# Kernel optimization log

Measured on AMD Instinct MI355X. Metric: run time of the kernel, lower is better.

The kernel has to match this reference:

```python
import jax, jax.numpy as jnp
import numpy as np

OC, IC = 11008, 4096
B, S = 32, 1
OUTLIER_FRACTION = 0.05


def setup_inputs() -> dict:
    key = jax.random.key(0)
    k1, k2, k3, k4 = jax.random.split(key, 4)
    x = jax.random.normal(k1, (B, S, IC), dtype=jnp.float32)
    weight = jax.random.normal(k2, (OC, IC), dtype=jnp.float32) * 0.02
    bias = jax.random.normal(k3, (OC,), dtype=jnp.float32) * 0.02
    outlier_mask = jax.random.uniform(k4, (OC, IC)) < OUTLIER_FRACTION
    return {"x": x, "weight": weight, "bias": bias, "outlier_mask": outlier_mask}


def _xnor_quant_weight(w, outlier_mask):
    # XnorBinaryLinear.quant_weight(outlier_mask=...): zero outliers, per-row
    # detached scale = mean|w|, center rows, sign() with STE clip path.
    wz = jnp.where(outlier_mask, 0.0, w)
    scale = jax.lax.stop_gradient(jnp.mean(jnp.abs(wz), axis=-1, keepdims=True))  # [OC,1]
    wc = wz - jnp.mean(wz, axis=-1, keepdims=True)  # centered rows
    clipped = jnp.clip(wc, -1.0, 1.0)
    # value = scale*sign(wc); gradient flows through clipped (STE)
    return jax.lax.stop_gradient(scale * jnp.sign(wc) - clipped) + clipped


def reference(x, weight, bias, outlier_mask):
    wq = _xnor_quant_weight(weight, outlier_mask)
    # binarize_except_outliers: keep full-precision weight at outlier positions
    w_eff = jnp.where(outlier_mask, weight, wq)  # [OC,IC]
    # F.linear(x, w, b) = x @ w.T + b
    return jnp.einsum("bsi,oi->bso", x, w_eff) + bias
```

## Files before the change

### kernel.cpp

```cpp
#include <hip/hip_runtime.h>
#include <stdint.h>


#define OC 11008
#define IC 4096
#define BATCH 32
#define SKM 8
#define SKF 4

typedef __attribute__((ext_vector_type(8))) short short8;
typedef __attribute__((ext_vector_type(4))) float floatx4;
typedef __attribute__((ext_vector_type(4))) int intx4;

static __device__ __forceinline__ unsigned short f2bf(float f) {
  uint32_t u = __builtin_bit_cast(uint32_t, f);
  uint32_t r = (u + 0x7fffu + ((u >> 16) & 1u)) >> 16;
  return (unsigned short)r;
}

__global__ __launch_bounds__(256) void fuse_kernel(
    const float* __restrict__ w, const int* __restrict__ mask,
    const float* __restrict__ x, unsigned short* __restrict__ weff,
    unsigned short* __restrict__ xbf) {
  const int blk = blockIdx.x;
  const int t = threadIdx.x;
  const int lane = t & 63;
  const int wvid = t >> 6;

  if (blk < 8) {
    const int b = blk * 4 + wvid;
    const float* xr = x + (size_t)b * IC;
    unsigned short* xo = xbf + (size_t)b * IC;
#pragma unroll
    for (int q = 0; q < 16; ++q) {
      const int i = (q << 8) + (lane << 2);
      const float4 v = *reinterpret_cast<const float4*>(xr + i);
      ushort4 u;
      u.x = f2bf(v.x); u.y = f2bf(v.y); u.z = f2bf(v.z); u.w = f2bf(v.w);
      *reinterpret_cast<ushort4*>(xo + i) = u;
    }
    return;
  }

  const int row = (blk - 8) * 4 + wvid;
  const float* wr = w + (size_t)row * IC;
  const int* mr = mask + (size_t)row * IC;

  float4 wv[16];
  uint32_t bits_lo = 0, bits_hi = 0;
  float s1 = 0.f, s2 = 0.f;
#pragma unroll
  for (int q = 0; q < 16; ++q) {
    const int i = (q << 8) + (lane << 2);
    wv[q] = *reinterpret_cast<const float4*>(wr + i);
    const intx4 mv =
        __builtin_nontemporal_load(reinterpret_cast<const intx4*>(mr + i));
    const uint32_t nb = (uint32_t)(mv.x != 0) | ((uint32_t)(mv.y != 0) << 1) |
                        ((uint32_t)(mv.z != 0) << 2) |
                        ((uint32_t)(mv.w != 0) << 3);
    if (q < 8)
      bits_lo |= nb << (q * 4);
    else
      bits_hi |= nb << ((q - 8) * 4);
    const float z0 = (nb & 1u) ? 0.f : wv[q].x;
    const float z1 = (nb & 2u) ? 0.f : wv[q].y;
    const float z2 = (nb & 4u) ? 0.f : wv[q].z;
    const float z3 = (nb & 8u) ? 0.f : wv[q].w;
    s1 += z0 + z1 + z2 + z3;
    s2 += fabsf(z0) + fabsf(z1) + fabsf(z2) + fabsf(z3);
  }

#pragma unroll
  for (int off = 1; off < 64; off <<= 1) {
    s1 += __shfl_xor(s1, off);
    s2 += __shfl_xor(s2, off);
  }
  const float mean = s1 * (1.0f / IC);
  const float scale = s2 * (1.0f / IC);

  unsigned short* wo = weff + (size_t)row * IC;
#pragma unroll
  for (int q = 0; q < 16; ++q) {
    const uint32_t nb =
        ((q < 8) ? (bits_lo >> (q * 4)) : (bits_hi >> ((q - 8) * 4))) & 0xFu;
    float4 v = wv[q];
    v.x = (nb & 1u) ? v.x : copysignf(scale, v.x - mean);
    v.y = (nb & 2u) ? v.y : copysignf(scale, v.y - mean);
    v.z = (nb & 4u) ? v.z : copysignf(scale, v.z - mean);
    v.w = (nb & 8u) ? v.w : copysignf(scale, v.w - mean);
    ushort4 u;
    u.x = f2bf(v.x); u.y = f2bf(v.y); u.z = f2bf(v.z); u.w = f2bf(v.w);
    *reinterpret_cast<ushort4*>(wo + (q << 8) + (lane << 2)) = u;
  }
}

__global__ __launch_bounds__(256) void mfma_kernel(
    const unsigned short* __restrict__ weff,
    const unsigned short* __restrict__ xbf, float* __restrict__ part) {
  const int bx = blockIdx.x;
  const int tile = bx >> 3;
  const int sk = bx & 7;
  const int t = threadIdx.x;
  const int wv = t >> 6;
  const int l = t & 63;
  const int l15 = l & 15, l4 = l >> 4;

  const int o = tile * 64 + wv * 16 + l15;
  const int k0 = sk * (IC / SKM) + l4 * 8;

  const unsigned short* bp = weff + (size_t)o * IC + k0;
  const unsigned short* ap0 = xbf + (size_t)l15 * IC + k0;
  const unsigned short* ap1 = xbf + (size_t)(16 + l15) * IC + k0;

  floatx4 acc0 = {0.f, 0.f, 0.f, 0.f};
  floatx4 acc1 = {0.f, 0.f, 0.f, 0.f};
#pragma unroll 4
  for (int kk = 0; kk < (IC / SKM) / 32; ++kk) {
    const short8 bf = *reinterpret_cast<const short8*>(bp + kk * 32);
    const short8 a0 = *reinterpret_cast<const short8*>(ap0 + kk * 32);
    const short8 a1 = *reinterpret_cast<const short8*>(ap1 + kk * 32);
    acc0 = __builtin_amdgcn_mfma_f32_16x16x32_bf16(a0, bf, acc0, 0, 0, 0);
    acc1 = __builtin_amdgcn_mfma_f32_16x16x32_bf16(a1, bf, acc1, 0, 0, 0);
  }

  float* pb = part + (size_t)sk * (BATCH * OC);
#pragma unroll
  for (int r = 0; r < 4; ++r) {
    const int b0 = l4 * 4 + r;
    pb[(size_t)b0 * OC + o] = acc0[r];
    pb[(size_t)(b0 + 16) * OC + o] = acc1[r];
  }
}

__global__ __launch_bounds__(256) void reduce_kernel(
    const float* __restrict__ part, const float* __restrict__ bias,
    float* __restrict__ out, int nsk) {
  const int idx = blockIdx.x * 256 + threadIdx.x;
  if (idx < BATCH * OC) {
    const int o = idx % OC;
    float v = bias[o];
    for (int sk = 0; sk < nsk; ++sk) v += part[(size_t)sk * (BATCH * OC) + idx];
    out[idx] = v;
  }
}

__global__ __launch_bounds__(256) void stats_kernel_fb(
    const int* __restrict__ mask, const float* __restrict__ w,
    float2* __restrict__ stats) {
  const int o = blockIdx.x;
  const int t = threadIdx.x;
  const float* wr = w + (size_t)o * IC;
  const int* mr = mask + (size_t)o * IC;
  float s1 = 0.f, s2 = 0.f;
#pragma unroll
  for (int q = 0; q < 4; ++q) {
    const int i = (q << 10) + (t << 2);
    const float4 wv = *reinterpret_cast<const float4*>(wr + i);
    const int4 mv = *reinterpret_cast<const int4*>(mr + i);
    const float z0 = mv.x ? 0.f : wv.x, z1 = mv.y ? 0.f : wv.y;
    const float z2 = mv.z ? 0.f : wv.z, z3 = mv.w ? 0.f : wv.w;
    s1 += z0 + z1 + z2 + z3;
    s2 += fabsf(z0) + fabsf(z1) + fabsf(z2) + fabsf(z3);
  }
#pragma unroll
  for (int off = 32; off > 0; off >>= 1) {
    s1 += __shfl_down(s1, off);
    s2 += __shfl_down(s2, off);
  }
  __shared__ float r1[4], r2[4];
  if ((t & 63) == 0) { r1[t >> 6] = s1; r2[t >> 6] = s2; }
  __syncthreads();
  if (t == 0)
    stats[o] = make_float2((r1[0] + r1[1] + r1[2] + r1[3]) * (1.0f / IC),
                           (r2[0] + r2[1] + r2[2] + r2[3]) * (1.0f / IC));
}

__global__ __launch_bounds__(256) void gemv_kernel_fb(
    const float* __restrict__ x, const float* __restrict__ w,
    const int* __restrict__ mask, const float2* __restrict__ stats,
    float* __restrict__ part) {
  const int bx = blockIdx.x;
  const int tile = bx >> 2;
  const int sk = bx & 3;
  const int t = threadIdx.x;
  const int wvid = t >> 6;
  const int lane = t & 63;
  const int il = lane & 15;
  const int bg = lane >> 4;
  const int row0 = tile * 32 + wvid * 8;
  const int i0 = sk * (IC / SKF);
  const float* wr0 = w + (size_t)row0 * IC;
  const int* mk0 = mask + (size_t)row0 * IC;
  const float* xb = x + (size_t)(bg * 8) * IC;

  float2 stv[8];
#pragma unroll
  for (int r = 0; r < 8; ++r) stv[r] = stats[row0 + r];
  float acc[8][8];
#pragma unroll
  for (int r = 0; r < 8; ++r)
#pragma unroll
    for (int j = 0; j < 8; ++j) acc[r][j] = 0.f;

  for (int s_ = 0; s_ < (IC / SKF) / 64; ++s_) {
    const int i = i0 + (s_ << 6) + (il << 2);
    float4 wf[8];
#pragma unroll
    for (int r = 0; r < 8; ++r) {
      wf[r] = *reinterpret_cast<const float4*>(wr0 + (size_t)r * IC + i);
      const int4 mv = *reinterpret_cast<const int4*>(mk0 + (size_t)r * IC + i);
      const float m = stv[r].x, sc = stv[r].y;
      wf[r].x = mv.x ? wf[r].x : copysignf(sc, wf[r].x - m);
      wf[r].y = mv.y ? wf[r].y : copysignf(sc, wf[r].y - m);
      wf[r].z = mv.z ? wf[r].z : copysignf(sc, wf[r].z - m);
      wf[r].w = mv.w ? wf[r].w : copysignf(sc, wf[r].w - m);
    }
#pragma unroll
    for (int j = 0; j < 8; ++j) {
      const float4 xv = *reinterpret_cast<const float4*>(xb + (size_t)j * IC + i);
#pragma unroll
      for (int r = 0; r < 8; ++r)
        acc[r][j] += wf[r].x * xv.x + wf[r].y * xv.y + wf[r].z * xv.z +
                     wf[r].w * xv.w;
    }
  }
#pragma unroll
  for (int off = 8; off >= 1; off >>= 1)
#pragma unroll
    for (int r = 0; r < 8; ++r)
#pragma unroll
      for (int j = 0; j < 8; ++j) acc[r][j] += __shfl_xor(acc[r][j], off);
  if (il == 0)
#pragma unroll
    for (int r = 0; r < 8; ++r)
#pragma unroll
      for (int j = 0; j < 8; ++j)
        part[(size_t)sk * (BATCH * OC) + (size_t)(bg * 8 + j) * OC +
             (row0 + r)] = acc[r][j];
}

extern "C" void kernel_launch(void* const* d_in, const int* in_sizes, int n_in,
                              void* d_out, int out_size, void* d_ws,
                              size_t ws_size, hipStream_t stream) {
  const float* x = (const float*)d_in[0];
  const float* w = (const float*)d_in[1];
  const float* bias = (const float*)d_in[2];
  const int* mask = (const int*)d_in[3];
  float* out = (float*)d_out;

  const size_t weff_b = (size_t)OC * IC * 2;
  const size_t xbf_b = (size_t)BATCH * IC * 2;
  const size_t part_b = (size_t)SKM * BATCH * OC * 4;

  if (ws_size >= weff_b + xbf_b + part_b) {
    unsigned short* weff = (unsigned short*)d_ws;
    unsigned short* xbf = (unsigned short*)((char*)d_ws + weff_b);
    float* part = (float*)((char*)d_ws + weff_b + xbf_b);

    fuse_kernel<<<8 + OC / 4, 256, 0, stream>>>(w, mask, x, weff, xbf);
    mfma_kernel<<<(OC / 64) * SKM, 256, 0, stream>>>(weff, xbf, part);
    reduce_kernel<<<(BATCH * OC + 255) / 256, 256, 0, stream>>>(part, bias, out,
                                                                SKM);
  } else {
    float2* stats = (float2*)d_ws;
    float* part = (float*)((char*)d_ws + (size_t)OC * sizeof(float2));
    stats_kernel_fb<<<OC, 256, 0, stream>>>(mask, w, stats);
    gemv_kernel_fb<<<(OC / 32) * SKF, 256, 0, stream>>>(x, w, mask, stats, part);
    reduce_kernel<<<(BATCH * OC + 255) / 256, 256, 0, stream>>>(part, bias, out,
                                                                SKF);
  }
}
```

Measured before the change: 112.4 us.

## Process one weight row per 1024-thread block with shared-memory row reduction

```diff
diff --git a/kernel.cpp b/kernel.cpp
--- a/kernel.cpp
+++ b/kernel.cpp
@@ -10,7 +10,6 @@
 
 typedef __attribute__((ext_vector_type(8))) short short8;
 typedef __attribute__((ext_vector_type(4))) float floatx4;
-typedef __attribute__((ext_vector_type(4))) int intx4;
 
 static __device__ __forceinline__ unsigned short f2bf(float f) {
   uint32_t u = __builtin_bit_cast(uint32_t, f);
@@ -18,80 +17,63 @@
   return (unsigned short)r;
 }
 
-__global__ __launch_bounds__(256) void fuse_kernel(
+__global__ __launch_bounds__(1024) void fuse_kernel(
     const float* __restrict__ w, const int* __restrict__ mask,
     const float* __restrict__ x, unsigned short* __restrict__ weff,
     unsigned short* __restrict__ xbf) {
   const int blk = blockIdx.x;
   const int t = threadIdx.x;
-  const int lane = t & 63;
-  const int wvid = t >> 6;
-
-  if (blk < 8) {
-    const int b = blk * 4 + wvid;
-    const float* xr = x + (size_t)b * IC;
-    unsigned short* xo = xbf + (size_t)b * IC;
-#pragma unroll
-    for (int q = 0; q < 16; ++q) {
-      const int i = (q << 8) + (lane << 2);
-      const float4 v = *reinterpret_cast<const float4*>(xr + i);
-      ushort4 u;
-      u.x = f2bf(v.x); u.y = f2bf(v.y); u.z = f2bf(v.z); u.w = f2bf(v.w);
-      *reinterpret_cast<ushort4*>(xo + i) = u;
-    }
+  const int i = t << 2;
+
+  if (blk < BATCH) {
+    const float* xr = x + (size_t)blk * IC;
+    unsigned short* xo = xbf + (size_t)blk * IC;
+    const float4 v = *reinterpret_cast<const float4*>(xr + i);
+    ushort4 u;
+    u.x = f2bf(v.x); u.y = f2bf(v.y); u.z = f2bf(v.z); u.w = f2bf(v.w);
+    *reinterpret_cast<ushort4*>(xo + i) = u;
     return;
   }
 
-  const int row = (blk - 8) * 4 + wvid;
+  const int row = blk - BATCH;
   const float* wr = w + (size_t)row * IC;
   const int* mr = mask + (size_t)row * IC;
 
-  float4 wv[16];
-  uint32_t bits_lo = 0, bits_hi = 0;
-  float s1 = 0.f, s2 = 0.f;
-#pragma unroll
-  for (int q = 0; q < 16; ++q) {
-    const int i = (q << 8) + (lane << 2);
-    wv[q] = *reinterpret_cast<const float4*>(wr + i);
-    const intx4 mv =
-        __builtin_nontemporal_load(reinterpret_cast<const intx4*>(mr + i));
-    const uint32_t nb = (uint32_t)(mv.x != 0) | ((uint32_t)(mv.y != 0) << 1) |
-                        ((uint32_t)(mv.z != 0) << 2) |
-                        ((uint32_t)(mv.w != 0) << 3);
-    if (q < 8)
-      bits_lo |= nb << (q * 4);
-    else
-      bits_hi |= nb << ((q - 8) * 4);
-    const float z0 = (nb & 1u) ? 0.f : wv[q].x;
-    const float z1 = (nb & 2u) ? 0.f : wv[q].y;
-    const float z2 = (nb & 4u) ? 0.f : wv[q].z;
-    const float z3 = (nb & 8u) ? 0.f : wv[q].w;
-    s1 += z0 + z1 + z2 + z3;
-    s2 += fabsf(z0) + fabsf(z1) + fabsf(z2) + fabsf(z3);
-  }
+  const float4 wv = *reinterpret_cast<const float4*>(wr + i);
+  const int4 mv = *reinterpret_cast<const int4*>(mr + i);
+  const uint32_t nb = (uint32_t)(mv.x != 0) | ((uint32_t)(mv.y != 0) << 1) |
+                      ((uint32_t)(mv.z != 0) << 2) |
+                      ((uint32_t)(mv.w != 0) << 3);
+  const float z0 = (nb & 1u) ? 0.f : wv.x;
+  const float z1 = (nb & 2u) ? 0.f : wv.y;
+  const float z2 = (nb & 4u) ? 0.f : wv.z;
+  const float z3 = (nb & 8u) ? 0.f : wv.w;
+  float s1 = z0 + z1 + z2 + z3;
+  float s2 = fabsf(z0) + fabsf(z1) + fabsf(z2) + fabsf(z3);
 
 #pragma unroll
   for (int off = 1; off < 64; off <<= 1) {
     s1 += __shfl_xor(s1, off);
     s2 += __shfl_xor(s2, off);
   }
-  const float mean = s1 * (1.0f / IC);
-  const float scale = s2 * (1.0f / IC);
-
-  unsigned short* wo = weff + (size_t)row * IC;
-#pragma unroll
-  for (int q = 0; q < 16; ++q) {
-    const uint32_t nb =
-        ((q < 8) ? (bits_lo >> (q * 4)) : (bits_hi >> ((q - 8) * 4))) & 0xFu;
-    float4 v = wv[q];
-    v.x = (nb & 1u) ? v.x : copysignf(scale, v.x - mean);
-    v.y = (nb & 2u) ? v.y : copysignf(scale, v.y - mean);
-    v.z = (nb & 4u) ? v.z : copysignf(scale, v.z - mean);
-    v.w = (nb & 8u) ? v.w : copysignf(scale, v.w - mean);
-    ushort4 u;
-    u.x = f2bf(v.x); u.y = f2bf(v.y); u.z = f2bf(v.z); u.w = f2bf(v.w);
-    *reinterpret_cast<ushort4*>(wo + (q << 8) + (lane << 2)) = u;
-  }
+  __shared__ float red[16][2];
+  const int wvid = t >> 6;
+  if ((t & 63) == 0) { red[wvid][0] = s1; red[wvid][1] = s2; }
+  __syncthreads();
+  float a = 0.f, b = 0.f;
+#pragma unroll
+  for (int k = 0; k < 16; ++k) { a += red[k][0]; b += red[k][1]; }
+  const float mean = a * (1.0f / IC);
+  const float scale = b * (1.0f / IC);
+
+  float4 v = wv;
+  v.x = (nb & 1u) ? v.x : copysignf(scale, v.x - mean);
+  v.y = (nb & 2u) ? v.y : copysignf(scale, v.y - mean);
+  v.z = (nb & 4u) ? v.z : copysignf(scale, v.z - mean);
+  v.w = (nb & 8u) ? v.w : copysignf(scale, v.w - mean);
+  ushort4 u;
+  u.x = f2bf(v.x); u.y = f2bf(v.y); u.z = f2bf(v.z); u.w = f2bf(v.w);
+  *reinterpret_cast<ushort4*>(weff + (size_t)row * IC + i) = u;
 }
 
 __global__ __launch_bounds__(256) void mfma_kernel(
@@ -257,7 +239,7 @@
     unsigned short* xbf = (unsigned short*)((char*)d_ws + weff_b);
     float* part = (float*)((char*)d_ws + weff_b + xbf_b);
 
-    fuse_kernel<<<8 + OC / 4, 256, 0, stream>>>(w, mask, x, weff, xbf);
+    fuse_kernel<<<BATCH + OC, 1024, 0, stream>>>(w, mask, x, weff, xbf);
     mfma_kernel<<<(OC / 64) * SKM, 256, 0, stream>>>(weff, xbf, part);
     reduce_kernel<<<(BATCH * OC + 255) / 256, 256, 0, stream>>>(part, bias, out,
                                                                 SKM);
```

Result: slower. 118.9 us (+5.8%).

## Split weight into packed sign bits plus sparse outlier corrections

Applied to the files above, without the earlier changes.

```diff
diff --git a/kernel.cpp b/kernel.cpp
--- a/kernel.cpp
+++ b/kernel.cpp
@@ -7,61 +7,75 @@
 #define BATCH 32
 #define SKM 8
 #define SKF 4
+#define CAP 512
 
 typedef __attribute__((ext_vector_type(8))) short short8;
 typedef __attribute__((ext_vector_type(4))) float floatx4;
-typedef __attribute__((ext_vector_type(4))) int intx4;
+typedef __attribute__((ext_vector_type(4))) unsigned int uintx4;
 
 static __device__ __forceinline__ unsigned short f2bf(float f) {
   uint32_t u = __builtin_bit_cast(uint32_t, f);
   uint32_t r = (u + 0x7fffu + ((u >> 16) & 1u)) >> 16;
   return (unsigned short)r;
 }
-
-__global__ __launch_bounds__(256) void fuse_kernel(
-    const float* __restrict__ w, const int* __restrict__ mask,
-    const float* __restrict__ x, unsigned short* __restrict__ weff,
-    unsigned short* __restrict__ xbf) {
+static __device__ __forceinline__ float bf2f(unsigned short h) {
+  uint32_t u = ((uint32_t)h) << 16;
+  return __builtin_bit_cast(float, u);
+}
+
+__global__ __launch_bounds__(256) void xprep_kernel(
+    const float* __restrict__ x, unsigned short* __restrict__ xbf,
+    unsigned short* __restrict__ xT) {
   const int blk = blockIdx.x;
   const int t = threadIdx.x;
-  const int lane = t & 63;
-  const int wvid = t >> 6;
-
-  if (blk < 8) {
-    const int b = blk * 4 + wvid;
+  if (blk < 64) {
+    const int i = blk * 64 + (t >> 2);
+    const int b0 = (t & 3) * 8;
+    unsigned short tmp[8];
+#pragma unroll
+    for (int j = 0; j < 8; ++j) tmp[j] = f2bf(x[(size_t)(b0 + j) * IC + i]);
+    *reinterpret_cast<short8*>(xT + (size_t)i * BATCH + b0) =
+        *reinterpret_cast<short8*>(tmp);
+  } else {
+    const int b = blk - 64;
     const float* xr = x + (size_t)b * IC;
     unsigned short* xo = xbf + (size_t)b * IC;
 #pragma unroll
-    for (int q = 0; q < 16; ++q) {
-      const int i = (q << 8) + (lane << 2);
+    for (int q = 0; q < 4; ++q) {
+      const int i = (q << 10) + (t << 2);
       const float4 v = *reinterpret_cast<const float4*>(xr + i);
       ushort4 u;
       u.x = f2bf(v.x); u.y = f2bf(v.y); u.z = f2bf(v.z); u.w = f2bf(v.w);
       *reinterpret_cast<ushort4*>(xo + i) = u;
     }
-    return;
-  }
-
-  const int row = (blk - 8) * 4 + wvid;
+  }
+}
+
+__global__ __launch_bounds__(256) void fuse2_kernel(
+    const float* __restrict__ w, const int* __restrict__ mask,
+    unsigned long long* __restrict__ signs, float* __restrict__ scaleArr,
+    int* __restrict__ countArr, uint32_t* __restrict__ corrArr) {
+  const int blk = blockIdx.x;
+  const int t = threadIdx.x;
+  const int lane = t & 63;
+  const int wvid = t >> 6;
+  const int row = blk * 4 + wvid;
+
   const float* wr = w + (size_t)row * IC;
   const int* mr = mask + (size_t)row * IC;
 
   float4 wv[16];
-  uint32_t bits_lo = 0, bits_hi = 0;
+  unsigned long long mb = 0;
   float s1 = 0.f, s2 = 0.f;
 #pragma unroll
   for (int q = 0; q < 16; ++q) {
     const int i = (q << 8) + (lane << 2);
     wv[q] = *reinterpret_cast<const float4*>(wr + i);
-    const intx4 mv =
-        __builtin_nontemporal_load(reinterpret_cast<const intx4*>(mr + i));
+    const int4 mv = *reinterpret_cast<const int4*>(mr + i);
     const uint32_t nb = (uint32_t)(mv.x != 0) | ((uint32_t)(mv.y != 0) << 1) |
                         ((uint32_t)(mv.z != 0) << 2) |
                         ((uint32_t)(mv.w != 0) << 3);
-    if (q < 8)
-      bits_lo |= nb << (q * 4);
-    else
-      bits_hi |= nb << ((q - 8) * 4);
+    mb |= (unsigned long long)nb << (q * 4);
     const float z0 = (nb & 1u) ? 0.f : wv[q].x;
     const float z1 = (nb & 2u) ? 0.f : wv[q].y;
     const float z2 = (nb & 4u) ? 0.f : wv[q].z;
@@ -77,26 +91,47 @@
   }
   const float mean = s1 * (1.0f / IC);
   const float scale = s2 * (1.0f / IC);
-
-  unsigned short* wo = weff + (size_t)row * IC;
+  if (lane == 0) scaleArr[row] = scale;
+
+  unsigned long long sb = 0;
 #pragma unroll
   for (int q = 0; q < 16; ++q) {
-    const uint32_t nb =
-        ((q < 8) ? (bits_lo >> (q * 4)) : (bits_hi >> ((q - 8) * 4))) & 0xFu;
-    float4 v = wv[q];
-    v.x = (nb & 1u) ? v.x : copysignf(scale, v.x - mean);
-    v.y = (nb & 2u) ? v.y : copysignf(scale, v.y - mean);
-    v.z = (nb & 4u) ? v.z : copysignf(scale, v.z - mean);
-    v.w = (nb & 8u) ? v.w : copysignf(scale, v.w - mean);
-    ushort4 u;
-    u.x = f2bf(v.x); u.y = f2bf(v.y); u.z = f2bf(v.z); u.w = f2bf(v.w);
-    *reinterpret_cast<ushort4*>(wo + (q << 8) + (lane << 2)) = u;
+    sb |= (unsigned long long)(wv[q].x < mean) << (q * 4 + 0);
+    sb |= (unsigned long long)(wv[q].y < mean) << (q * 4 + 1);
+    sb |= (unsigned long long)(wv[q].z < mean) << (q * 4 + 2);
+    sb |= (unsigned long long)(wv[q].w < mean) << (q * 4 + 3);
+  }
+  signs[(size_t)row * 64 + lane] = sb;
+
+  int cnt = __popcll(mb);
+  int pref = cnt;
+#pragma unroll
+  for (int d = 1; d < 64; d <<= 1) {
+    int v = __shfl_up(pref, d);
+    if (lane >= d) pref += v;
+  }
+  if (lane == 63) countArr[row] = (pref < CAP) ? pref : CAP;
+  int pos = pref - cnt;
+  unsigned long long mm = mb;
+  while (mm) {
+    const int b = __ffsll(mm) - 1;
+    mm &= mm - 1;
+    const int q = b >> 2, e = b & 3;
+    const int idx = (q << 8) + (lane << 2) + e;
+    const float val = wr[idx];
+    const float sg = (val < mean) ? -scale : scale;
+    const float corr = val - sg;
+    if (pos < CAP)
+      corrArr[(size_t)row * CAP + pos] =
+          ((uint32_t)idx << 16) | (uint32_t)f2bf(corr);
+    ++pos;
   }
 }
 
 __global__ __launch_bounds__(256) void mfma_kernel(
-    const unsigned short* __restrict__ weff,
-    const unsigned short* __restrict__ xbf, float* __restrict__ part) {
+    const unsigned long long* __restrict__ signs,
+    const float* __restrict__ scaleArr, const unsigned short* __restrict__ xbf,
+    float* __restrict__ part) {
   const int bx = blockIdx.x;
   const int tile = bx >> 3;
   const int sk = bx & 7;
@@ -108,15 +143,29 @@
   const int o = tile * 64 + wv * 16 + l15;
   const int k0 = sk * (IC / SKM) + l4 * 8;
 
-  const unsigned short* bp = weff + (size_t)o * IC + k0;
+  const unsigned long long* sgp = signs + (size_t)o * 64;
   const unsigned short* ap0 = xbf + (size_t)l15 * IC + k0;
   const unsigned short* ap1 = xbf + (size_t)(16 + l15) * IC + k0;
+  const float scl = scaleArr[o];
 
   floatx4 acc0 = {0.f, 0.f, 0.f, 0.f};
   floatx4 acc1 = {0.f, 0.f, 0.f, 0.f};
-#pragma unroll 4
-  for (int kk = 0; kk < (IC / SKM) / 32; ++kk) {
-    const short8 bf = *reinterpret_cast<const short8*>(bp + kk * 32);
+#pragma unroll
+  for (int kk = 0; kk < 16; ++kk) {
+    const int k = k0 + kk * 32;
+    const int l_src = (k & 255) >> 2;
+    const int sh = (k >> 8) * 4;
+    const unsigned long long s0 = sgp[l_src];
+    const unsigned long long s1v = sgp[l_src + 1];
+    const uint32_t bits8 = ((uint32_t)(s0 >> sh) & 0xFu) |
+                           (((uint32_t)(s1v >> sh) & 0xFu) << 4);
+    uintx4 pr;
+#pragma unroll
+    for (int p = 0; p < 4; ++p) {
+      pr[p] = (((bits8 >> (2 * p)) & 1u) ? 0xBF80u : 0x3F80u) |
+              (((bits8 >> (2 * p + 1)) & 1u) ? 0xBF800000u : 0x3F800000u);
+    }
+    const short8 bf = __builtin_bit_cast(short8, pr);
     const short8 a0 = *reinterpret_cast<const short8*>(ap0 + kk * 32);
     const short8 a1 = *reinterpret_cast<const short8*>(ap1 + kk * 32);
     acc0 = __builtin_amdgcn_mfma_f32_16x16x32_bf16(a0, bf, acc0, 0, 0, 0);
@@ -127,8 +176,49 @@
 #pragma unroll
   for (int r = 0; r < 4; ++r) {
     const int b0 = l4 * 4 + r;
-    pb[(size_t)b0 * OC + o] = acc0[r];
-    pb[(size_t)(b0 + 16) * OC + o] = acc1[r];
+    pb[(size_t)b0 * OC + o] = acc0[r] * scl;
+    pb[(size_t)(b0 + 16) * OC + o] = acc1[r] * scl;
+  }
+}
+
+__global__ __launch_bounds__(256) void sparse_kernel(
+    const uint32_t* __restrict__ corrArr, const int* __restrict__ countArr,
+    const unsigned short* __restrict__ xT, float* __restrict__ part) {
+  __shared__ float lds[4][64][33];
+  const int t = threadIdx.x;
+  const int lane = t & 63;
+  const int wvid = t >> 6;
+  const int row = blockIdx.x * 4 + wvid;
+
+  const int cnt = countArr[row];
+  float acc[32];
+#pragma unroll
+  for (int b = 0; b < 32; ++b) acc[b] = 0.f;
+
+  for (int j = lane; j < cnt; j += 64) {
+    const uint32_t p = corrArr[(size_t)row * CAP + j];
+    const int idx = p >> 16;
+    const float cv = bf2f((unsigned short)(p & 0xFFFFu));
+    const unsigned short* xr = xT + (size_t)idx * BATCH;
+    const short8 h0 = *reinterpret_cast<const short8*>(xr);
+    const short8 h1 = *reinterpret_cast<const short8*>(xr + 8);
+    const short8 h2 = *reinterpret_cast<const short8*>(xr + 16);
+    const short8 h3 = *reinterpret_cast<const short8*>(xr + 24);
+#pragma unroll
+    for (int e = 0; e < 8; ++e) {
+      acc[e] += cv * bf2f((unsigned short)h0[e]);
+      acc[8 + e] += cv * bf2f((unsigned short)h1[e]);
+      acc[16 + e] += cv * bf2f((unsigned short)h2[e]);
+      acc[24 + e] += cv * bf2f((unsigned short)h3[e]);
+    }
+  }
+
+#pragma unroll
+  for (int b = 0; b < 32; ++b) lds[wvid][lane][b] = acc[b];
+  if (lane < 32) {
+    float s = 0.f;
+    for (int l2 = 0; l2 < 64; ++l2) s += lds[wvid][l2][lane];
+    part[(size_t)SKM * (BATCH * OC) + (size_t)lane * OC + row] = s;
   }
 }
 
@@ -248,19 +338,33 @@
   const int* mask = (const int*)d_in[3];
   float* out = (float*)d_out;
 
-  const size_t weff_b = (size_t)OC * IC * 2;
+  const size_t scale_b = (size_t)OC * 4;
+  const size_t count_b = (size_t)OC * 4;
+  const size_t signs_b = (size_t)OC * 64 * 8;
+  const size_t corr_b = (size_t)OC * CAP * 4;
   const size_t xbf_b = (size_t)BATCH * IC * 2;
-  const size_t part_b = (size_t)SKM * BATCH * OC * 4;
-
-  if (ws_size >= weff_b + xbf_b + part_b) {
-    unsigned short* weff = (unsigned short*)d_ws;
-    unsigned short* xbf = (unsigned short*)((char*)d_ws + weff_b);
-    float* part = (float*)((char*)d_ws + weff_b + xbf_b);
-
-    fuse_kernel<<<8 + OC / 4, 256, 0, stream>>>(w, mask, x, weff, xbf);
-    mfma_kernel<<<(OC / 64) * SKM, 256, 0, stream>>>(weff, xbf, part);
+  const size_t xT_b = (size_t)IC * BATCH * 2;
+  const size_t part_b = (size_t)(SKM + 1) * BATCH * OC * 4;
+  const size_t need = scale_b + count_b + signs_b + corr_b + xbf_b + xT_b + part_b;
+
+  if (ws_size >= need) {
+    char* p = (char*)d_ws;
+    float* scaleArr = (float*)p;                 p += scale_b;
+    int* countArr = (int*)p;                     p += count_b;
+    unsigned long long* signs = (unsigned long long*)p; p += signs_b;
+    uint32_t* corrArr = (uint32_t*)p;            p += corr_b;
+    unsigned short* xbf = (unsigned short*)p;    p += xbf_b;
+    unsigned short* xT = (unsigned short*)p;     p += xT_b;
+    float* part = (float*)p;
+
+    xprep_kernel<<<96, 256, 0, stream>>>(x, xbf, xT);
+    fuse2_kernel<<<OC / 4, 256, 0, stream>>>(w, mask, signs, scaleArr,
+                                             countArr, corrArr);
+    mfma_kernel<<<(OC / 64) * SKM, 256, 0, stream>>>(signs, scaleArr, xbf,
+                                                     part);
+    sparse_kernel<<<OC / 4, 256, 0, stream>>>(corrArr, countArr, xT, part);
     reduce_kernel<<<(BATCH * OC + 255) / 256, 256, 0, stream>>>(part, bias, out,
-                                                                SKM);
+                                                                SKM + 1);
   } else {
     float2* stats = (float2*)d_ws;
     float* part = (float*)((char*)d_ws + (size_t)OC * sizeof(float2));
```

After: 162.5 us. 44.6% more time.
